# Kernel optimization log

Hardware: AMD Instinct MI355X
Metric: run time of the kernel (lower is better)

## Reference

```python
import jax, jax.numpy as jnp
import numpy as np

N_KNOTS = 16
D_LATENT = 32
DEGREE = 3
GRID = (256, 256, 256)


def _de_boor(x, t, c, degree):
    """Vectorized de Boor B-spline evaluation.
    x: [...] query points; t: [n_knots+6] padded knots; c: [n_knots+2] control points."""
    k = jnp.digitize(x, t) - 1  # [...] int32 segment index per query point
    d = [c[j + k - degree] for j in range(degree + 1)]  # degree+1 gathers, each shaped like x
    for r in range(1, degree + 1):
        for j in range(degree, r - 1, -1):
            t_lo = t[j + k - degree]
            t_hi = t[j + 1 + k - r]
            alpha = (x - t_lo) / (t_hi - t_lo)
            d[j] = (1.0 - alpha) * d[j - 1] + alpha * d[j]
    return d[degree]


def setup_inputs() -> dict:
    key = jax.random.key(0)
    ks = jax.random.split(key, 6)
    d, n = D_LATENT, N_KNOTS
    s = lambda m: 1.0 / np.sqrt(m)
    return {
        "x": jax.random.uniform(ks[0], GRID, jnp.float32, 0.0, 1.7),  # |k| grid, fftfreq-normalized
        "a": jax.random.uniform(ks[1], (1,), jnp.float32, 0.1, 1.0),  # scale factor
        "W1": jax.random.normal(ks[2], (1, d), jnp.float32),
        "b1": jnp.zeros((d,), jnp.float32),
        "W2": jax.random.normal(ks[3], (d, d), jnp.float32) * s(d),
        "b2": jnp.zeros((d,), jnp.float32),
        "Ww": jax.random.normal(ks[4], (d, n + 1), jnp.float32) * s(d),
        "bw": jnp.zeros((n + 1,), jnp.float32),
        "Wk": jax.random.normal(ks[5], (d, n - 1), jnp.float32) * s(d),
        "bk": jnp.zeros((n - 1,), jnp.float32),
    }


def reference(x, a, W1, b1, W2, b2, Ww, bw, Wk, bk):
    # tiny sin-MLP on the scalar scale factor a
    net = jnp.sin(a @ W1 + b1)          # [d_latent]
    net = jnp.sin(net @ W2 + b2)        # [d_latent]
    w = net @ Ww + bw                   # [n_knots+1] control-point deltas
    k = net @ Wk + bk                   # [n_knots-1] knot logits
    # monotone knot positions in (0,1], prepend 0
    k = jnp.concatenate([jnp.zeros((1,), x.dtype), jnp.cumsum(jax.nn.softmax(k))])
    w = jnp.concatenate([jnp.zeros((1,), x.dtype), w])  # [n_knots+2] control points
    # pad knots for degree-3 spline: 3 zeros, internal knots, 3 ones
    ak = jnp.concatenate([jnp.zeros((3,), x.dtype), k, jnp.ones((3,), x.dtype)])
    xc = jnp.clip(x / jnp.sqrt(jnp.asarray(3.0, x.dtype)), 0.0, 1.0 - 1e-4)
    return _de_boor(xc, ak, w, DEGREE)
```

## Files before the change

kernel.cpp:

```cpp
#include <hip/hip_runtime.h>
#include <math.h>


typedef float fvec4 __attribute__((ext_vector_type(4)));

__device__ __forceinline__ float deboor_eval(float x, int k, const float* t, const float* c) {
    float d[4];
#pragma unroll
    for (int j = 0; j < 4; ++j) d[j] = c[j + k - 3];
#pragma unroll
    for (int r = 1; r <= 3; ++r) {
#pragma unroll
        for (int j = 3; j >= 1; --j) {
            if (j < r) continue;
            float tlo = t[j + k - 3];
            float thi = t[j + 1 + k - r];
            float al = (x - tlo) / (thi - tlo);
            d[j] = (1.0f - al) * d[j - 1] + al * d[j];
        }
    }
    return d[3];
}

__global__ void spline_setup_kernel(
    const float* __restrict__ a,  const float* __restrict__ W1, const float* __restrict__ b1,
    const float* __restrict__ W2, const float* __restrict__ b2,
    const float* __restrict__ Ww, const float* __restrict__ bw,
    const float* __restrict__ Wk, const float* __restrict__ bk,
    float* __restrict__ ws)
{
    __shared__ float net1[32], net2[32], cpt[18], kl[15], ak[22];
    int t = threadIdx.x;
    float av = a[0];

    if (t < 32) net1[t] = sinf(av * W1[t] + b1[t]);
    __syncthreads();

    if (t < 32) {
        float s = b2[t];
#pragma unroll
        for (int i = 0; i < 32; ++i) s += net1[i] * W2[i * 32 + t];
        net2[t] = sinf(s);
    }
    __syncthreads();

    if (t < 17) {
        float s = bw[t];
#pragma unroll
        for (int i = 0; i < 32; ++i) s += net2[i] * Ww[i * 17 + t];
        cpt[t + 1] = s;
    }
    if (t == 63) cpt[0] = 0.0f;
    if (t >= 32 && t < 47) {
        int j = t - 32;
        float s = bk[j];
#pragma unroll
        for (int i = 0; i < 32; ++i) s += net2[i] * Wk[i * 15 + j];
        kl[j] = s;
    }
    __syncthreads();

    if (t == 0) {
        float m = kl[0];
        for (int j = 1; j < 15; ++j) m = fmaxf(m, kl[j]);
        float e[15], sum = 0.0f;
        for (int j = 0; j < 15; ++j) { e[j] = expf(kl[j] - m); sum += e[j]; }
        float inv = 1.0f / sum;
        ak[0] = ak[1] = ak[2] = 0.0f;
        ak[3] = 0.0f;
        float cum = 0.0f;
        for (int j = 0; j < 15; ++j) { cum += e[j]; ak[4 + j] = cum * inv; }
        ak[19] = ak[20] = ak[21] = 1.0f;
    }
    __syncthreads();

    if (t < 14) ws[t] = ak[4 + t];

    if (t < 15) {
        int k = t + 3;
        float t0 = ak[k], t1 = ak[k + 1];
        float dl = (t1 - t0) * (1.0f / 3.0f);
        float f0 = deboor_eval(t0,              k, ak, cpt);
        float f1 = deboor_eval(t0 + dl,         k, ak, cpt);
        float f2 = deboor_eval(t0 + 2.0f * dl,  k, ak, cpt);
        float f3 = deboor_eval(t0 + 3.0f * dl,  k, ak, cpt);
        float idl  = 1.0f / dl;
        float g01  = (f1 - f0) * idl, g12 = (f2 - f1) * idl, g23 = (f3 - f2) * idl;
        float h012 = (g12 - g01) * (0.5f * idl), h123 = (g23 - g12) * (0.5f * idl);
        float q    = (h123 - h012) * (idl * (1.0f / 3.0f));
        float c0 = f0;
        float c1 = g01 - dl * h012 + 2.0f * dl * dl * q;
        float c2 = h012 - 3.0f * dl * q;
        float c3 = q;
        ws[16 + t] = t0;
        ws[32 + 4 * t + 0] = c0;
        ws[32 + 4 * t + 1] = c1;
        ws[32 + 4 * t + 2] = c2;
        ws[32 + 4 * t + 3] = c3;
    }
}

__global__ __launch_bounds__(256) void spline_eval_kernel(
    const float* __restrict__ x, const float* __restrict__ p,
    float* __restrict__ out, int n)
{
    __shared__ float  sStart[16];
    __shared__ fvec4  sC[16];
    int t = threadIdx.x;
    if (t < 15) {
        sStart[t] = p[16 + t];
        sC[t]     = ((const fvec4*)(p + 32))[t];
    }
    float bb[14];
#pragma unroll
    for (int j = 0; j < 14; ++j) bb[j] = p[j];
    __syncthreads();

    const float kInvSqrt3 = 0.57735026918962576f;
    const float kXMax     = 1.0f - 1e-4f;

    int n4 = n >> 2;
    int gtid = blockIdx.x * blockDim.x + t;
    int stride = gridDim.x * blockDim.x;
    const fvec4* x4 = (const fvec4*)x;
    fvec4* o4 = (fvec4*)out;

    for (int i = gtid; i < n4; i += stride) {
        fvec4 xv = __builtin_nontemporal_load(&x4[i]);
        float rr[4];
#pragma unroll
        for (int e = 0; e < 4; ++e) {
            float xc = fminf(fmaxf(xv[e] * kInvSqrt3, 0.0f), kXMax);
            int s = 0;
#pragma unroll
            for (int j = 0; j < 14; ++j) s += (xc >= bb[j]) ? 1 : 0;
            fvec4 c = sC[s];
            float u = xc - sStart[s];
            rr[e] = fmaf(fmaf(fmaf(c.w, u, c.z), u, c.y), u, c.x);
        }
        fvec4 r; r.x = rr[0]; r.y = rr[1]; r.z = rr[2]; r.w = rr[3];
        __builtin_nontemporal_store(r, &o4[i]);
    }
    for (int i = (n4 << 2) + gtid; i < n; i += stride) {
        float xc = fminf(fmaxf(x[i] * kInvSqrt3, 0.0f), kXMax);
        int s = 0;
#pragma unroll
        for (int j = 0; j < 14; ++j) s += (xc >= bb[j]) ? 1 : 0;
        fvec4 c = sC[s];
        float u = xc - sStart[s];
        out[i] = fmaf(fmaf(fmaf(c.w, u, c.z), u, c.y), u, c.x);
    }
}

extern "C" void kernel_launch(void* const* d_in, const int* in_sizes, int n_in,
                              void* d_out, int out_size, void* d_ws, size_t ws_size,
                              hipStream_t stream)
{
    const float* x  = (const float*)d_in[0];
    const float* a  = (const float*)d_in[1];
    const float* W1 = (const float*)d_in[2];
    const float* b1 = (const float*)d_in[3];
    const float* W2 = (const float*)d_in[4];
    const float* b2 = (const float*)d_in[5];
    const float* Ww = (const float*)d_in[6];
    const float* bw = (const float*)d_in[7];
    const float* Wk = (const float*)d_in[8];
    const float* bk = (const float*)d_in[9];
    float* ws  = (float*)d_ws;
    float* out = (float*)d_out;

    spline_setup_kernel<<<1, 64, 0, stream>>>(a, W1, b1, W2, b2, Ww, bw, Wk, bk, ws);
    spline_eval_kernel<<<2048, 256, 0, stream>>>(x, ws, out, out_size);
}
```

Measured before the change: 139.7 us.

## Fuse spline setup into eval kernel, recomputing coefficients per block

Merges the single-block setup kernel into the main evaluation kernel, so each of the 2048 blocks recomputes the MLP, softmax knots and per-segment cubic coefficients into shared memory. This removes one kernel launch and the workspace round trip, along with the serialization between the two kernels. In exchange, every block repeats the serial setup work (several syncs, a single-thread softmax loop, de Boor evaluations) before it can stream x, which adds latency at the start of each block.

After: 138.8 us. Within noise of the previous version (-0.7%).

```diff
diff --git a/kernel.cpp b/kernel.cpp
--- a/kernel.cpp
+++ b/kernel.cpp
@@ -22,18 +22,22 @@
     return d[3];
 }
 
-__global__ void spline_setup_kernel(
+__global__ __launch_bounds__(256) void spline_fused_kernel(
+    const float* __restrict__ x,
     const float* __restrict__ a,  const float* __restrict__ W1, const float* __restrict__ b1,
     const float* __restrict__ W2, const float* __restrict__ b2,
     const float* __restrict__ Ww, const float* __restrict__ bw,
     const float* __restrict__ Wk, const float* __restrict__ bk,
-    float* __restrict__ ws)
+    float* __restrict__ out, int n)
 {
     __shared__ float net1[32], net2[32], cpt[18], kl[15], ak[22];
+    __shared__ float sBB[14];
+    __shared__ float sStart[16];
+    __shared__ fvec4 sC[16];
+
     int t = threadIdx.x;
-    float av = a[0];
 
-    if (t < 32) net1[t] = sinf(av * W1[t] + b1[t]);
+    if (t < 32) net1[t] = sinf(a[0] * W1[t] + b1[t]);
     __syncthreads();
 
     if (t < 32) {
@@ -74,8 +78,7 @@
     }
     __syncthreads();
 
-    if (t < 14) ws[t] = ak[4 + t];
-
+    if (t < 14) sBB[t] = ak[4 + t];
     if (t < 15) {
         int k = t + 3;
         float t0 = ak[k], t1 = ak[k + 1];
@@ -88,33 +91,19 @@
         float g01  = (f1 - f0) * idl, g12 = (f2 - f1) * idl, g23 = (f3 - f2) * idl;
         float h012 = (g12 - g01) * (0.5f * idl), h123 = (g23 - g12) * (0.5f * idl);
         float q    = (h123 - h012) * (idl * (1.0f / 3.0f));
-        float c0 = f0;
-        float c1 = g01 - dl * h012 + 2.0f * dl * dl * q;
-        float c2 = h012 - 3.0f * dl * q;
-        float c3 = q;
-        ws[16 + t] = t0;
-        ws[32 + 4 * t + 0] = c0;
-        ws[32 + 4 * t + 1] = c1;
-        ws[32 + 4 * t + 2] = c2;
-        ws[32 + 4 * t + 3] = c3;
+        fvec4 c;
+        c.x = f0;
+        c.y = g01 - dl * h012 + 2.0f * dl * dl * q;
+        c.z = h012 - 3.0f * dl * q;
+        c.w = q;
+        sStart[t] = t0;
+        sC[t] = c;
     }
-}
+    __syncthreads();
 
-__global__ __launch_bounds__(256) void spline_eval_kernel(
-    const float* __restrict__ x, const float* __restrict__ p,
-    float* __restrict__ out, int n)
-{
-    __shared__ float  sStart[16];
-    __shared__ fvec4  sC[16];
-    int t = threadIdx.x;
-    if (t < 15) {
-        sStart[t] = p[16 + t];
-        sC[t]     = ((const fvec4*)(p + 32))[t];
-    }
     float bb[14];
 #pragma unroll
-    for (int j = 0; j < 14; ++j) bb[j] = p[j];
-    __syncthreads();
+    for (int j = 0; j < 14; ++j) bb[j] = sBB[j];
 
     const float kInvSqrt3 = 0.57735026918962576f;
     const float kXMax     = 1.0f - 1e-4f;
@@ -166,9 +155,8 @@
     const float* bw = (const float*)d_in[7];
     const float* Wk = (const float*)d_in[8];
     const float* bk = (const float*)d_in[9];
-    float* ws  = (float*)d_ws;
     float* out = (float*)d_out;
 
-    spline_setup_kernel<<<1, 64, 0, stream>>>(a, W1, b1, W2, b2, Ww, bw, Wk, bk, ws);
-    spline_eval_kernel<<<2048, 256, 0, stream>>>(x, ws, out, out_size);
+    spline_fused_kernel<<<2048, 256, 0, stream>>>(
+        x, a, W1, b1, W2, b2, Ww, bw, Wk, bk, out, out_size);
 }
```
